# Performance work log

Hardware: AMD Instinct MI355X
Metric: run time of the kernel (lower is better)

## Reference

```python
import jax, jax.numpy as jnp
import numpy as np

NPG = 400          # nodes per graph (CC400 atlas ROIs)
B = 512            # graphs per batch
N = B * NPG        # total nodes
EPG = 6400         # edges per graph (avg degree 16)
E = B * EPG
F_IN = 200         # node feature dim
H = 64             # hidden_channels
C = 2              # num_classes


def _lin(k, fi, fo):
    return jax.random.normal(k, (fi, fo), jnp.float32) / np.sqrt(fi)


def setup_inputs() -> dict:
    key = jax.random.key(0)
    ks = jax.random.split(key, 16)
    # intra-graph edges: local src/dst in [0, NPG) plus per-graph offset
    g = jnp.repeat(jnp.arange(B, dtype=jnp.int32), EPG)
    src = jax.random.randint(ks[0], (E,), 0, NPG, dtype=jnp.int32) + g * NPG
    dst = jax.random.randint(ks[1], (E,), 0, NPG, dtype=jnp.int32) + g * NPG
    edge_index = jnp.stack([src, dst])  # [2, E]
    x = jax.random.normal(ks[2], (N, F_IN), jnp.float32)
    return dict(
        x=x, edge_index=edge_index, npg=NPG,
        # SAGEConv i: out = lin_l(mean_agg) + lin_r(x); lin_l carries the bias
        W1l=_lin(ks[3], F_IN, H), W1r=_lin(ks[4], F_IN, H), b1=jnp.zeros((H,), jnp.float32),
        W2l=_lin(ks[5], H, H), W2r=_lin(ks[6], H, H), b2=jnp.zeros((H,), jnp.float32),
        W3l=_lin(ks[7], H, H), W3r=_lin(ks[8], H, H), b3=jnp.zeros((H,), jnp.float32),
        # SAGPooling score GNN = GraphConv(H, 1): lin_rel(sum_agg) + lin_root(x)
        Wpr=_lin(ks[9], H, 1), bpr=jnp.zeros((1,), jnp.float32), Wpo=_lin(ks[10], H, 1),
        # final classifier
        Wlin=_lin(ks[11], H, C), blin=jnp.zeros((C,), jnp.float32),
    )


def reference(x, edge_index, npg, W1l, W1r, b1, W2l, W2r, b2, W3l, W3r, b3,
              Wpr, bpr, Wpo, Wlin, blin):
    n = x.shape[0]
    src, dst = edge_index[0], edge_index[1]

    deg = jax.ops.segment_sum(jnp.ones((src.shape[0],), x.dtype), dst, num_segments=n)
    inv_deg = 1.0 / jnp.maximum(deg, 1.0)  # [n]

    def sage(h, Wl, Wr, b):
        # mean aggregation over incoming edges, then lin_l(agg)+b + lin_r(h)
        agg = jax.ops.segment_sum(h[src], dst, num_segments=n) * inv_deg[:, None]
        return agg @ Wl + b + h @ Wr

    x1 = jax.nn.relu(sage(x, W1l, W1r, b1))
    x2 = jax.nn.relu(sage(x1, W2l, W2r, b2)) + x1
    x3 = jax.nn.relu(sage(x2, W3l, W3r, b3)) + x2

    # SAGPooling score via GraphConv (add aggregation)
    score = (jax.ops.segment_sum(x3[src], dst, num_segments=n) @ Wpr + bpr
             + x3 @ Wpo)[:, 0]  # [n]

    nb = n // npg            # number of graphs
    k = npg // 2             # ratio = 0.5, uniform graph sizes
    vals, idx = jax.lax.top_k(score.reshape(nb, npg), k)       # [nb, k]
    flat_idx = (jnp.arange(nb, dtype=idx.dtype)[:, None] * npg + idx).reshape(-1)
    xp = x3[flat_idx] * jnp.tanh(vals.reshape(-1))[:, None]    # [nb*k, H]

    pooled = xp.reshape(nb, k, -1).mean(axis=1)                # global_mean_pool
    logits = pooled @ Wlin + blin
    return jax.nn.log_softmax(logits, axis=1)
```

## Files before the change

### kernel.cpp

```cpp
#include <hip/hip_runtime.h>
#include <hip/hip_bf16.h>
#include <math.h>

#define F_IN 200
#define HDIM 64
#define NPG  400
#define EPG  6400
#define KSEL 200

typedef __attribute__((ext_vector_type(4))) float f32x4;
typedef __attribute__((ext_vector_type(8))) short s16x8;

__device__ __forceinline__ void gload_lds16(const void* g, void* l) {
    __builtin_amdgcn_global_load_lds(
        (const __attribute__((address_space(1))) void*)g,
        (__attribute__((address_space(3))) void*)l, 16, 0, 0);
}

__device__ __forceinline__ unsigned int bf16_rne(float x) {
    unsigned int b = __float_as_uint(x);
    return (b + 0x7FFFu + ((b >> 16) & 1u)) >> 16;
}

__device__ __forceinline__ void split8(f32x4 v0, f32x4 v1, s16x8& h, s16x8& l) {
    float x[8] = {v0.x, v0.y, v0.z, v0.w, v1.x, v1.y, v1.z, v1.w};
#pragma unroll
    for (int j = 0; j < 8; j++) {
        unsigned int hb = bf16_rne(x[j]);
        float hf = __uint_as_float(hb << 16);
        float r = x[j] - hf;
        unsigned int lb = bf16_rne(r);
        h[j] = (short)hb;
        l[j] = (short)lb;
    }
}

__global__ void pack_wf(const float* __restrict__ Wl, const float* __restrict__ Wr,
                        short* __restrict__ WF, int K, int KC) {
    int idx = blockIdx.x * blockDim.x + threadIdx.x;
    if (idx >= KC * 4096) return;
    int j    = idx & 7;
    int lane = (idx >> 3) & 63;
    int nf   = (idx >> 9) & 7;
    int kc   = idx >> 12;
    int k = kc * 32 + (lane >> 4) * 8 + j;
    int n = nf * 16 + (lane & 15);
    float v = 0.f;
    if (k < K) v = (n < 64) ? Wl[k * 64 + n] : Wr[k * 64 + (n - 64)];
    unsigned int hb = bf16_rne(v);
    float hf = __uint_as_float(hb << 16);
    unsigned int lb = bf16_rne(v - hf);
    WF[(size_t)((kc * 8 + nf) * 2 + 0) * 512 + lane * 8 + j] = (short)hb;
    WF[(size_t)((kc * 8 + nf) * 2 + 1) * 512 + lane * 8 + j] = (short)lb;
}

template <int K, int LDX, int KC, int TAIL>
__global__ __launch_bounds__(256) void gemm_lds(const float* __restrict__ X,
                                                const short* __restrict__ WF,
                                                float* __restrict__ O) {
    __shared__ float Xs[2][128 * 32];
    __shared__ short Ws[2][8 * 2 * 512];
    const int tid  = threadIdx.x;
    const int lane = tid & 63;
    const int wave = tid >> 6;
    const size_t rowbase = (size_t)blockIdx.x * 128;
    const f32x4 zero4 = (f32x4){0.f, 0.f, 0.f, 0.f};

    const int srow_off = wave * 32 + (lane >> 3);
    const int sbyte    = 16 * ((lane & 7) ^ (lane >> 3));

#define DMA_CHUNK(b, kc_) {                                                      \
    _Pragma("unroll")                                                            \
    for (int j = 0; j < 4; j++) {                                                \
        const char* xsrc = (const char*)X +                                      \
            (rowbase + srow_off + j * 8) * (size_t)(LDX * 4) + (kc_) * 128 + sbyte; \
        gload_lds16(xsrc, (char*)&Xs[b][0] + wave * 4096 + j * 1024);            \
        const short* wsrc = WF + (size_t)(kc_) * 8192 + wave * 2048 + j * 512 + lane * 8; \
        gload_lds16(wsrc, (char*)&Ws[b][0] + wave * 4096 + j * 1024);            \
    } }

    f32x4 acc[2][8];
#pragma unroll
    for (int m = 0; m < 2; m++)
#pragma unroll
        for (int nf = 0; nf < 8; nf++) acc[m][nf] = zero4;

    DMA_CHUNK(0, 0);
    __syncthreads();

    for (int kc = 0; kc < KC; kc++) {
        const int b = kc & 1;
        if (kc + 1 < KC) DMA_CHUNK(b ^ 1, kc + 1);

        s16x8 ah[2], al[2];
#pragma unroll
        for (int m = 0; m < 2; m++) {
            const int lr = wave * 32 + m * 16 + (lane & 15);
            const int g0 = (lane >> 4) * 2;
            f32x4 v0 = *(const f32x4*)&Xs[b][lr * 32 + 4 * (g0 ^ (lane & 7))];
            f32x4 v1 = *(const f32x4*)&Xs[b][lr * 32 + 4 * ((g0 + 1) ^ (lane & 7))];
            split8(v0, v1, ah[m], al[m]);
        }
#pragma unroll
        for (int nf = 0; nf < 8; nf++) {
            s16x8 wh = *(const s16x8*)&Ws[b][(nf * 2 + 0) * 512 + lane * 8];
            s16x8 wl = *(const s16x8*)&Ws[b][(nf * 2 + 1) * 512 + lane * 8];
#pragma unroll
            for (int m = 0; m < 2; m++) {
                acc[m][nf] = __builtin_amdgcn_mfma_f32_16x16x32_bf16(ah[m], wh, acc[m][nf], 0, 0, 0);
                acc[m][nf] = __builtin_amdgcn_mfma_f32_16x16x32_bf16(al[m], wh, acc[m][nf], 0, 0, 0);
                acc[m][nf] = __builtin_amdgcn_mfma_f32_16x16x32_bf16(ah[m], wl, acc[m][nf], 0, 0, 0);
            }
        }
        __syncthreads();
    }
#undef DMA_CHUNK

    if constexpr (TAIL > 0) {
        s16x8 ah[2], al[2];
#pragma unroll
        for (int m = 0; m < 2; m++) {
            const size_t row = rowbase + wave * 32 + m * 16 + (lane & 15);
            const int k0 = KC * 32 + (lane >> 4) * 8;
            f32x4 v0 = (k0 + 4 <= K) ? *(const f32x4*)&X[row * (size_t)LDX + k0] : zero4;
            f32x4 v1 = (k0 + 8 <= K) ? *(const f32x4*)&X[row * (size_t)LDX + k0 + 4] : zero4;
            split8(v0, v1, ah[m], al[m]);
        }
#pragma unroll
        for (int nf = 0; nf < 8; nf++) {
            s16x8 wh = *(const s16x8*)&WF[(size_t)((KC * 8 + nf) * 2 + 0) * 512 + lane * 8];
            s16x8 wl = *(const s16x8*)&WF[(size_t)((KC * 8 + nf) * 2 + 1) * 512 + lane * 8];
#pragma unroll
            for (int m = 0; m < 2; m++) {
                acc[m][nf] = __builtin_amdgcn_mfma_f32_16x16x32_bf16(ah[m], wh, acc[m][nf], 0, 0, 0);
                acc[m][nf] = __builtin_amdgcn_mfma_f32_16x16x32_bf16(al[m], wh, acc[m][nf], 0, 0, 0);
                acc[m][nf] = __builtin_amdgcn_mfma_f32_16x16x32_bf16(ah[m], wl, acc[m][nf], 0, 0, 0);
            }
        }
    }

    float* cs0 = &Xs[0][wave * 1024];
    float* cs1 = &Xs[1][wave * 1024];
#pragma unroll
    for (int m = 0; m < 2; m++) {
        const int scol = lane & 15;
        const int srow = (lane >> 4) * 4;
#pragma unroll
        for (int nf = 0; nf < 8; nf++)
#pragma unroll
            for (int r = 0; r < 4; r++) {
                int cr = srow + r;
                float* p = (cr < 8) ? cs0 + cr * 128 : cs1 + (cr - 8) * 128;
                p[nf * 16 + scol] = acc[m][nf][r];
            }
#pragma unroll
        for (int ps = 0; ps < 8; ps++) {
            int row = ps * 2 + (lane >> 5);
            const float* p = (row < 8) ? cs0 + row * 128 : cs1 + (row - 8) * 128;
            f32x4 v = *(const f32x4*)&p[(lane & 31) * 4];
            *(f32x4*)&O[(rowbase + wave * 32 + m * 16 + row) * 128 + (lane & 31) * 4] = v;
        }
    }
}

__global__ __launch_bounds__(256) void csr_build(
    const int* __restrict__ esrc, const int* __restrict__ edst,
    int* __restrict__ csr_src, int* __restrict__ rowptr,
    int* __restrict__ degs, float* __restrict__ invdeg)
{
    __shared__ int cnt[NPG];
    __shared__ int off[NPG];
    __shared__ int cur[NPG];
    const int g = blockIdx.x, tid = threadIdx.x;
    const int ebase = g * EPG, nodebase = g * NPG;
    for (int i = tid; i < NPG; i += 256) cnt[i] = 0;
    __syncthreads();
    for (int e = tid; e < EPG; e += 256)
        atomicAdd(&cnt[edst[ebase + e] - nodebase], 1);
    __syncthreads();
    if (tid == 0) {
        int run = 0;
        for (int i = 0; i < NPG; i++) { off[i] = run; run += cnt[i]; }
    }
    __syncthreads();
    for (int i = tid; i < NPG; i += 256) {
        cur[i] = off[i];
        rowptr[nodebase + i] = off[i];
        degs[nodebase + i] = cnt[i];
        invdeg[nodebase + i] = 1.f / fmaxf((float)cnt[i], 1.f);
    }
    __syncthreads();
    for (int e = tid; e < EPG; e += 256) {
        int ld = edst[ebase + e] - nodebase;
        int p = atomicAdd(&cur[ld], 1);
        csr_src[ebase + p] = esrc[ebase + e] - nodebase;
    }
}

__global__ __launch_bounds__(1024) void agg_lds(
    const float* __restrict__ A,
    const int* __restrict__ csr_src, const int* __restrict__ rowptr,
    const int* __restrict__ degs, const float* __restrict__ invdeg,
    const float* __restrict__ bias,
    const float* __restrict__ resid,
    float* __restrict__ Xout)
{
    __shared__ float y[NPG * 64];
    __shared__ int   csr_l[EPG];
    const int g = blockIdx.x, tid = threadIdx.x;
    const int ebase = g * EPG, nodebase = g * NPG;

    for (int idx = tid; idx < NPG * 16; idx += 1024) {
        int node = idx >> 4, c4 = (idx & 15) * 4;
        *(float4*)&y[node * 64 + c4] =
            *(const float4*)&A[(size_t)(nodebase + node) * 128 + c4];
    }
    for (int e = tid; e < EPG; e += 1024) csr_l[e] = csr_src[ebase + e];
    __syncthreads();

    const int wave = tid >> 6, lane = tid & 63;
    for (int node = wave; node < NPG; node += 16) {
        const int start = rowptr[nodebase + node];
        const int dg = degs[nodebase + node];
        float acc = 0.f;
        int j = 0;
        for (; j + 4 <= dg; j += 4) {
            int s0 = csr_l[start + j];
            int s1 = csr_l[start + j + 1];
            int s2 = csr_l[start + j + 2];
            int s3 = csr_l[start + j + 3];
            acc += y[s0 * 64 + lane] + y[s1 * 64 + lane]
                 + y[s2 * 64 + lane] + y[s3 * 64 + lane];
        }
        for (; j < dg; j++) acc += y[csr_l[start + j] * 64 + lane];

        float v = acc * invdeg[nodebase + node] + bias[lane]
                + A[(size_t)(nodebase + node) * 128 + 64 + lane];
        v = fmaxf(v, 0.f);
        if (resid) v += resid[(size_t)(nodebase + node) * 64 + lane];
        Xout[(size_t)(nodebase + node) * 64 + lane] = v;
    }
}

__global__ __launch_bounds__(256) void score_pool(
    const float* __restrict__ X3,
    const int* __restrict__ esrc, const int* __restrict__ edst,
    const float* __restrict__ Wpr, const float* __restrict__ bpr,
    const float* __restrict__ Wpo,
    const float* __restrict__ Wlin, const float* __restrict__ blin,
    float* __restrict__ out)
{
    __shared__ float t0[NPG], s[NPG], w[NPG];
    __shared__ float wpr[64], wpo[64];
    __shared__ float pp[4 * 64];
    __shared__ float pooled[64];
    __shared__ float lg[2];
    const int g = blockIdx.x, tid = threadIdx.x;
    if (tid < 64) { wpr[tid] = Wpr[tid]; wpo[tid] = Wpo[tid]; }
    __syncthreads();

    const int nodebase = g * NPG;
    for (int i = tid; i < NPG; i += 256) {
        const float* xr = &X3[(size_t)(nodebase + i) * 64];
        float a0 = 0.f, a1 = 0.f;
        for (int d = 0; d < 64; d++) { float x = xr[d]; a0 += x * wpr[d]; a1 += x * wpo[d]; }
        t0[i] = a0;
        s[i] = bpr[0] + a1;
    }
    __syncthreads();
    const int ebase = g * EPG;
    for (int e = tid; e < EPG; e += 256) {
        int ls = esrc[ebase + e] - nodebase;
        int ld = edst[ebase + e] - nodebase;
        atomicAdd(&s[ld], t0[ls]);
    }
    __syncthreads();
    for (int i = tid; i < NPG; i += 256) {
        float si = s[i];
        int cnt = 0;
        for (int j = 0; j < NPG; j++) {
            float sj = s[j];
            cnt += (sj > si) || (sj == si && j < i);
        }
        w[i] = (cnt < KSEL) ? tanhf(si) * (1.f / KSEL) : 0.f;
    }
    __syncthreads();
    const int d = tid & 63, part = tid >> 6;
    float acc = 0.f;
    for (int i = part * 100; i < part * 100 + 100; i++)
        acc += w[i] * X3[(size_t)(nodebase + i) * 64 + d];
    pp[part * 64 + d] = acc;
    __syncthreads();
    if (tid < 64) pooled[tid] = pp[tid] + pp[64 + tid] + pp[128 + tid] + pp[192 + tid];
    __syncthreads();
    if (tid < 2) {
        float l = blin[tid];
        for (int dd = 0; dd < 64; dd++) l += pooled[dd] * Wlin[dd * 2 + tid];
        lg[tid] = l;
    }
    __syncthreads();
    if (tid < 2) {
        float m = fmaxf(lg[0], lg[1]);
        float lse = m + logf(expf(lg[0] - m) + expf(lg[1] - m));
        out[g * 2 + tid] = lg[tid] - lse;
    }
}

extern "C" void kernel_launch(void* const* d_in, const int* in_sizes, int n_in,
                              void* d_out, int out_size, void* d_ws, size_t ws_size,
                              hipStream_t stream) {
    const float* x    = (const float*)d_in[0];
    const int*   eidx = (const int*)d_in[1];
    const float* W1l  = (const float*)d_in[3];
    const float* W1r  = (const float*)d_in[4];
    const float* b1   = (const float*)d_in[5];
    const float* W2l  = (const float*)d_in[6];
    const float* W2r  = (const float*)d_in[7];
    const float* b2   = (const float*)d_in[8];
    const float* W3l  = (const float*)d_in[9];
    const float* W3r  = (const float*)d_in[10];
    const float* b3   = (const float*)d_in[11];
    const float* Wpr  = (const float*)d_in[12];
    const float* bpr  = (const float*)d_in[13];
    const float* Wpo  = (const float*)d_in[14];
    const float* Wlin = (const float*)d_in[15];
    const float* blin = (const float*)d_in[16];

    const int N = in_sizes[0] / F_IN;
    const int E = in_sizes[1] / 2;
    const int B = N / NPG;
    const int* esrc = eidx;
    const int* edst = eidx + E;

    float* ws = (float*)d_ws;
    float* A      = ws;
    float* P0     = A + (size_t)N * 128;
    float* P1     = P0 + (size_t)N * 64;
    float* invdeg = P1 + (size_t)N * 64;
    short* WF1    = (short*)(invdeg + N);
    short* WF2    = WF1 + 57344;
    short* WF3    = WF2 + 16384;
    int*   csr    = (int*)(WF3 + 16384);
    int*   rowptr = csr + E;
    int*   degs   = rowptr + N;

    pack_wf<<<(7 * 4096 + 255) / 256, 256, 0, stream>>>(W1l, W1r, WF1, 200, 7);
    pack_wf<<<(2 * 4096 + 255) / 256, 256, 0, stream>>>(W2l, W2r, WF2, 64, 2);
    pack_wf<<<(2 * 4096 + 255) / 256, 256, 0, stream>>>(W3l, W3r, WF3, 64, 2);

    csr_build<<<B, 256, 0, stream>>>(esrc, edst, csr, rowptr, degs, invdeg);

    gemm_lds<200, 200, 6, 8><<<N / 128, 256, 0, stream>>>(x, WF1, A);
    agg_lds<<<B, 1024, 0, stream>>>(A, csr, rowptr, degs, invdeg, b1, nullptr, P0);

    gemm_lds<64, 64, 2, 0><<<N / 128, 256, 0, stream>>>(P0, WF2, A);
    agg_lds<<<B, 1024, 0, stream>>>(A, csr, rowptr, degs, invdeg, b2, P0, P1);

    gemm_lds<64, 64, 2, 0><<<N / 128, 256, 0, stream>>>(P1, WF3, A);
    agg_lds<<<B, 1024, 0, stream>>>(A, csr, rowptr, degs, invdeg, b3, P1, P0);

    score_pool<<<B, 256, 0, stream>>>(P0, esrc, edst, Wpr, bpr, Wpo, Wlin, blin,
                                      (float*)d_out);
}
```

Before: 479.5 us.

## Aggregate-then-transform for layers 2-3 with fused concat GEMM epilogue

For the 64-wide layers, mean aggregation now runs on the input features first, and a new combine GEMM multiplies the concatenated [agg | h] (K=128) by stacked [Wl; Wr]. Bias, ReLU and the residual are applied in the GEMM epilogue, so the 128-wide intermediate is no longer written and re-read. This reduces memory traffic per layer (64-wide outputs instead of 128-wide A) at the cost of an extra M buffer round trip. The new GEMM uses 1024-thread blocks of 256 rows.

```diff
diff --git a/kernel.cpp b/kernel.cpp
--- a/kernel.cpp
+++ b/kernel.cpp
@@ -54,6 +54,24 @@
     WF[(size_t)((kc * 8 + nf) * 2 + 1) * 512 + lane * 8 + j] = (short)lb;
 }
 
+__global__ void pack_wf4(const float* __restrict__ Wl, const float* __restrict__ Wr,
+                         short* __restrict__ WF) {
+    int idx = blockIdx.x * blockDim.x + threadIdx.x;
+    if (idx >= 4 * 2048) return;
+    int j    = idx & 7;
+    int lane = (idx >> 3) & 63;
+    int nf   = (idx >> 9) & 3;
+    int kc   = idx >> 11;
+    int k = kc * 32 + (lane >> 4) * 8 + j;
+    int n = nf * 16 + (lane & 15);
+    float v = (k < 64) ? Wl[k * 64 + n] : Wr[(k - 64) * 64 + n];
+    unsigned int hb = bf16_rne(v);
+    float hf = __uint_as_float(hb << 16);
+    unsigned int lb = bf16_rne(v - hf);
+    WF[(size_t)((kc * 4 + nf) * 2 + 0) * 512 + lane * 8 + j] = (short)hb;
+    WF[(size_t)((kc * 4 + nf) * 2 + 1) * 512 + lane * 8 + j] = (short)lb;
+}
+
 template <int K, int LDX, int KC, int TAIL>
 __global__ __launch_bounds__(256) void gemm_lds(const float* __restrict__ X,
                                                 const short* __restrict__ WF,
@@ -163,6 +181,93 @@
     }
 }
 
+__global__ __launch_bounds__(1024) void combine_gemm(
+    const float* __restrict__ M, const float* __restrict__ H,
+    const short* __restrict__ WF, const float* __restrict__ bias,
+    const float* __restrict__ resid, float* __restrict__ P)
+{
+    __shared__ float Xs[2][256 * 32];
+    __shared__ short Ws[2][4 * 2 * 512];
+    const int tid  = threadIdx.x;
+    const int lane = tid & 63;
+    const int wave = tid >> 6;
+    const size_t rowbase = (size_t)blockIdx.x * 256;
+
+#define DMA_C(b, c_) {                                                           \
+    const float* srcbuf_ = ((c_) < 2) ? M : H;                                   \
+    _Pragma("unroll")                                                            \
+    for (int i = 0; i < 2; i++) {                                                \
+        int rr = i * 8 + (lane >> 3);                                            \
+        int jj = (lane & 7) ^ (rr & 7);                                          \
+        const char* src = (const char*)(srcbuf_ + (rowbase + wave * 16 + rr) * 64) \
+                          + ((c_) & 1) * 128 + jj * 16;                          \
+        gload_lds16(src, (char*)&Xs[b][0] + wave * 2048 + i * 1024 + lane * 16); \
+    }                                                                            \
+    if (tid < 512) {                                                             \
+        const short* wsrc = WF + (size_t)(c_) * 4096 + tid * 8;                  \
+        gload_lds16(wsrc, (char*)&Ws[b][0] + tid * 16);                          \
+    } }
+
+    f32x4 acc[4];
+#pragma unroll
+    for (int nf = 0; nf < 4; nf++) acc[nf] = (f32x4){0.f, 0.f, 0.f, 0.f};
+
+    DMA_C(0, 0);
+    __syncthreads();
+
+    for (int c = 0; c < 4; c++) {
+        const int b = c & 1;
+        if (c + 1 < 4) DMA_C(b ^ 1, c + 1);
+
+        const int r = lane & 15;
+        const int j0 = (lane >> 4) * 2;
+        const float* abase = &Xs[b][wave * 512 + r * 32];
+        f32x4 v0 = *(const f32x4*)&abase[((j0    ) ^ (r & 7)) * 4];
+        f32x4 v1 = *(const f32x4*)&abase[((j0 + 1) ^ (r & 7)) * 4];
+        s16x8 ah, al;
+        split8(v0, v1, ah, al);
+#pragma unroll
+        for (int nf = 0; nf < 4; nf++) {
+            s16x8 wh = *(const s16x8*)&Ws[b][(nf * 2 + 0) * 512 + lane * 8];
+            s16x8 wl = *(const s16x8*)&Ws[b][(nf * 2 + 1) * 512 + lane * 8];
+            acc[nf] = __builtin_amdgcn_mfma_f32_16x16x32_bf16(ah, wh, acc[nf], 0, 0, 0);
+            acc[nf] = __builtin_amdgcn_mfma_f32_16x16x32_bf16(al, wh, acc[nf], 0, 0, 0);
+            acc[nf] = __builtin_amdgcn_mfma_f32_16x16x32_bf16(ah, wl, acc[nf], 0, 0, 0);
+        }
+        __syncthreads();
+    }
+#undef DMA_C
+
+    {
+        const int scol = lane & 15;
+        const int srow = (lane >> 4) * 4;
+#pragma unroll
+        for (int nf = 0; nf < 4; nf++)
+#pragma unroll
+            for (int ri = 0; ri < 4; ri++) {
+                int cr = srow + ri;
+                float* p = (cr < 8) ? &Xs[0][wave * 512 + cr * 64]
+                                    : &Xs[1][wave * 512 + (cr - 8) * 64];
+                p[nf * 16 + scol] = acc[nf][ri];
+            }
+#pragma unroll
+        for (int i = 0; i < 4; i++) {
+            int row = i * 4 + (lane >> 4);
+            int col = (lane & 15) * 4;
+            const float* p = (row < 8) ? &Xs[0][wave * 512 + row * 64]
+                                       : &Xs[1][wave * 512 + (row - 8) * 64];
+            f32x4 v = *(const f32x4*)&p[col];
+            size_t grow = rowbase + wave * 16 + row;
+            f32x4 bb = *(const f32x4*)&bias[col];
+            f32x4 rr = *(const f32x4*)&resid[grow * 64 + col];
+            f32x4 o;
+#pragma unroll
+            for (int q = 0; q < 4; q++) o[q] = fmaxf(v[q] + bb[q], 0.f) + rr[q];
+            *(f32x4*)&P[grow * 64 + col] = o;
+        }
+    }
+}
+
 __global__ __launch_bounds__(256) void csr_build(
     const int* __restrict__ esrc, const int* __restrict__ edst,
     int* __restrict__ csr_src, int* __restrict__ rowptr,
@@ -202,7 +307,6 @@
     const int* __restrict__ csr_src, const int* __restrict__ rowptr,
     const int* __restrict__ degs, const float* __restrict__ invdeg,
     const float* __restrict__ bias,
-    const float* __restrict__ resid,
     float* __restrict__ Xout)
 {
     __shared__ float y[NPG * 64];
@@ -236,9 +340,46 @@
 
         float v = acc * invdeg[nodebase + node] + bias[lane]
                 + A[(size_t)(nodebase + node) * 128 + 64 + lane];
-        v = fmaxf(v, 0.f);
-        if (resid) v += resid[(size_t)(nodebase + node) * 64 + lane];
-        Xout[(size_t)(nodebase + node) * 64 + lane] = v;
+        Xout[(size_t)(nodebase + node) * 64 + lane] = fmaxf(v, 0.f);
+    }
+}
+
+__global__ __launch_bounds__(1024) void agg_in(
+    const float* __restrict__ H,
+    const int* __restrict__ csr_src, const int* __restrict__ rowptr,
+    const int* __restrict__ degs, const float* __restrict__ invdeg,
+    float* __restrict__ M)
+{
+    __shared__ float y[NPG * 64];
+    __shared__ int   csr_l[EPG];
+    const int g = blockIdx.x, tid = threadIdx.x;
+    const int ebase = g * EPG, nodebase = g * NPG;
+
+    for (int idx = tid; idx < NPG * 16; idx += 1024) {
+        int node = idx >> 4, c4 = (idx & 15) * 4;
+        *(float4*)&y[node * 64 + c4] =
+            *(const float4*)&H[(size_t)(nodebase + node) * 64 + c4];
+    }
+    for (int e = tid; e < EPG; e += 1024) csr_l[e] = csr_src[ebase + e];
+    __syncthreads();
+
+    const int wave = tid >> 6, lane = tid & 63;
+    for (int node = wave; node < NPG; node += 16) {
+        const int start = rowptr[nodebase + node];
+        const int dg = degs[nodebase + node];
+        float acc = 0.f;
+        int j = 0;
+        for (; j + 4 <= dg; j += 4) {
+            int s0 = csr_l[start + j];
+            int s1 = csr_l[start + j + 1];
+            int s2 = csr_l[start + j + 2];
+            int s3 = csr_l[start + j + 3];
+            acc += y[s0 * 64 + lane] + y[s1 * 64 + lane]
+                 + y[s2 * 64 + lane] + y[s3 * 64 + lane];
+        }
+        for (; j < dg; j++) acc += y[csr_l[start + j] * 64 + lane];
+
+        M[(size_t)(nodebase + node) * 64 + lane] = acc * invdeg[nodebase + node];
     }
 }
 
@@ -336,28 +477,29 @@
     float* A      = ws;
     float* P0     = A + (size_t)N * 128;
     float* P1     = P0 + (size_t)N * 64;
-    float* invdeg = P1 + (size_t)N * 64;
+    float* Mb     = P1 + (size_t)N * 64;
+    float* invdeg = Mb + (size_t)N * 64;
     short* WF1    = (short*)(invdeg + N);
-    short* WF2    = WF1 + 57344;
-    short* WF3    = WF2 + 16384;
-    int*   csr    = (int*)(WF3 + 16384);
+    short* WFc2   = WF1 + 57344;
+    short* WFc3   = WFc2 + 16384;
+    int*   csr    = (int*)(WFc3 + 16384);
     int*   rowptr = csr + E;
     int*   degs   = rowptr + N;
 
     pack_wf<<<(7 * 4096 + 255) / 256, 256, 0, stream>>>(W1l, W1r, WF1, 200, 7);
-    pack_wf<<<(2 * 4096 + 255) / 256, 256, 0, stream>>>(W2l, W2r, WF2, 64, 2);
-    pack_wf<<<(2 * 4096 + 255) / 256, 256, 0, stream>>>(W3l, W3r, WF3, 64, 2);
+    pack_wf4<<<(4 * 2048 + 255) / 256, 256, 0, stream>>>(W2l, W2r, WFc2);
+    pack_wf4<<<(4 * 2048 + 255) / 256, 256, 0, stream>>>(W3l, W3r, WFc3);
 
     csr_build<<<B, 256, 0, stream>>>(esrc, edst, csr, rowptr, degs, invdeg);
 
     gemm_lds<200, 200, 6, 8><<<N / 128, 256, 0, stream>>>(x, WF1, A);
-    agg_lds<<<B, 1024, 0, stream>>>(A, csr, rowptr, degs, invdeg, b1, nullptr, P0);
-
-    gemm_lds<64, 64, 2, 0><<<N / 128, 256, 0, stream>>>(P0, WF2, A);
-    agg_lds<<<B, 1024, 0, stream>>>(A, csr, rowptr, degs, invdeg, b2, P0, P1);
-
-    gemm_lds<64, 64, 2, 0><<<N / 128, 256, 0, stream>>>(P1, WF3, A);
-    agg_lds<<<B, 1024, 0, stream>>>(A, csr, rowptr, degs, invdeg, b3, P1, P0);
+    agg_lds<<<B, 1024, 0, stream>>>(A, csr, rowptr, degs, invdeg, b1, P0);
+
+    agg_in<<<B, 1024, 0, stream>>>(P0, csr, rowptr, degs, invdeg, Mb);
+    combine_gemm<<<N / 256, 1024, 0, stream>>>(Mb, P0, WFc2, b2, P0, P1);
+
+    agg_in<<<B, 1024, 0, stream>>>(P1, csr, rowptr, degs, invdeg, Mb);
+    combine_gemm<<<N / 256, 1024, 0, stream>>>(Mb, P1, WFc3, b3, P1, P0);
 
     score_pool<<<B, 256, 0, stream>>>(P0, esrc, edst, Wpr, bpr, Wpo, Wlin, blin,
                                       (float*)d_out);
```

After: 466.0 us. 1.03x faster.
